# Kernel optimization log

Measured on AMD Instinct MI355X. Metric: run time of the kernel, lower is better.

## Reference

```python
import jax, jax.numpy as jnp
import numpy as np


def setup_inputs() -> dict:
    key = jax.random.key(0)
    k1, k2, k3, k4, k5 = jax.random.split(key, 5)
    B, C, H, W = 8, 256, 64, 64
    Cp = C // 8  # query/key channels
    x = jax.random.normal(k1, (B, C, H, W), dtype=jnp.float32)
    # 1x1 conv weights (bias=False in the module), spectral norm treated as a fixed weight scale
    Wq = jax.random.normal(k2, (Cp, C), dtype=jnp.float32) * 0.05
    Wk = jax.random.normal(k3, (Cp, C), dtype=jnp.float32) * 0.05
    Wv = jax.random.normal(k4, (C, C), dtype=jnp.float32) * 0.05
    gamma = jax.random.normal(k5, (1,), dtype=jnp.float32)
    return {"x": x, "Wq": Wq, "Wk": Wk, "Wv": Wv, "gamma": gamma}


def reference(x, Wq, Wk, Wv, gamma):
    B, C, H, W = x.shape
    xf = x.reshape(B, C, H * W)  # (B, C, N)
    # ConvLayer = 1x1 conv (no bias) followed by ReLU
    f = jax.nn.relu(jnp.einsum('oc,bcn->bon', Wq, xf))  # (B, C', N)
    g = jax.nn.relu(jnp.einsum('oc,bcn->bon', Wk, xf))  # (B, C', N)
    h = jax.nn.relu(jnp.einsum('oc,bcn->bon', Wv, xf))  # (B, C, N)
    # beta = softmax(f^T g, dim=1): normalize over the FIRST N axis (faithful to source)
    scores = jnp.einsum('bcn,bcm->bnm', f, g)  # (B, N, N)
    beta = jax.nn.softmax(scores, axis=1)
    o = gamma * jnp.einsum('bcn,bnm->bcm', h, beta) + xf  # (B, C, N)
    return o.reshape(B, C, H, W)
```

## Files before the change

kernel.cpp:

```cpp
#include <hip/hip_runtime.h>


typedef __attribute__((ext_vector_type(8))) short bf16x8;
typedef __attribute__((ext_vector_type(4))) float f32x4;
typedef __attribute__((ext_vector_type(4))) unsigned short us4;

#define LOG2E 1.44269504088896f

static __device__ __forceinline__ unsigned short f2bf(float x) {
    union { float f; unsigned u; } v; v.f = x;
    unsigned r = v.u + 0x7FFFu + ((v.u >> 16) & 1u);
    return (unsigned short)(r >> 16);
}
static __device__ __forceinline__ float bf2f(unsigned short u) {
    union { unsigned u; float f; } v; v.u = ((unsigned)u) << 16;
    return v.f;
}

__global__ __launch_bounds__(256) void wconv_kernel(
    const float* __restrict__ Wq, const float* __restrict__ Wk,
    const float* __restrict__ Wv, unsigned short* __restrict__ wq,
    unsigned short* __restrict__ wk, unsigned short* __restrict__ wv)
{
    const int i = blockIdx.x * 256 + threadIdx.x;
    if (i < 8192)            wq[i] = f2bf(Wq[i] * LOG2E);
    else if (i < 16384)      wk[i - 8192] = f2bf(Wk[i - 8192]);
    else                     wv[i - 16384] = f2bf(Wv[i - 16384]);
}

#define XPITCH 264
#define HPITCH 72
__global__ __launch_bounds__(256, 2) void producer_kernel(
    const float* __restrict__ x, const unsigned short* __restrict__ wq,
    const unsigned short* __restrict__ wk, const unsigned short* __restrict__ wv,
    unsigned short* __restrict__ f_t, unsigned short* __restrict__ g_t,
    unsigned short* __restrict__ h_bf, float* __restrict__ normg,
    float* __restrict__ pmax)
{
    __shared__ unsigned short xh_s[256 * HPITCH];
    __shared__ unsigned short fg_s[4 * 2 * 512];

    const int tid  = threadIdx.x;
    const int w    = tid >> 6;
    const int lane = tid & 63;
    const int q    = lane >> 4;
    const int r    = lane & 15;
    const int b    = blockIdx.x & 7;
    const int nt   = blockIdx.x >> 3;
    const int n0   = nt << 6;
    const size_t bN = (size_t)b << 12;
    const f32x4 zero = {0.f, 0.f, 0.f, 0.f};

#pragma unroll
    for (int jj = 0; jj < 4; jj++) {
        const int task = jj * 256 + tid;
        const int n4 = task & 15;
        const int c4 = task >> 4;
        float va[4][4];
#pragma unroll
        for (int i = 0; i < 4; i++) {
            const f32x4 v = __builtin_nontemporal_load(
                (const f32x4*)(x + ((size_t)b << 20)
                               + (size_t)(c4 * 4 + i) * 4096 + n0) + n4);
            va[i][0] = v.x; va[i][1] = v.y; va[i][2] = v.z; va[i][3] = v.w;
        }
#pragma unroll
        for (int i = 0; i < 4; i++) {
            us4 t;
            t.x = f2bf(va[0][i]); t.y = f2bf(va[1][i]);
            t.z = f2bf(va[2][i]); t.w = f2bf(va[3][i]);
            *(us4*)(xh_s + (n4 * 4 + i) * XPITCH + c4 * 4) = t;
        }
    }
    __syncthreads();

    f32x4 acch[4][4];
    f32x4 accf[2], accg[2];
#pragma unroll
    for (int cs = 0; cs < 4; cs++)
#pragma unroll
        for (int ns = 0; ns < 4; ns++) acch[cs][ns] = zero;
    accf[0] = accf[1] = accg[0] = accg[1] = zero;

    for (int ks = 0; ks < 8; ks++) {
        const int kof = ks * 32 + q * 8;
        bf16x8 av[4], aq[2], ak[2];
#pragma unroll
        for (int cs = 0; cs < 4; cs++)
            av[cs] = *(const bf16x8*)(wv + (size_t)(w * 64 + cs * 16 + r) * 256 + kof);
#pragma unroll
        for (int ms = 0; ms < 2; ms++) {
            aq[ms] = *(const bf16x8*)(wq + (size_t)(ms * 16 + r) * 256 + kof);
            ak[ms] = *(const bf16x8*)(wk + (size_t)(ms * 16 + r) * 256 + kof);
        }
#pragma unroll
        for (int ns = 0; ns < 4; ns++) {
            const bf16x8 bx = *(const bf16x8*)(xh_s + (ns * 16 + r) * XPITCH + kof);
#pragma unroll
            for (int cs = 0; cs < 4; cs++)
                acch[cs][ns] = __builtin_amdgcn_mfma_f32_16x16x32_bf16(av[cs], bx, acch[cs][ns], 0, 0, 0);
            if (ns == w) {
#pragma unroll
                for (int ms = 0; ms < 2; ms++) {
                    accf[ms] = __builtin_amdgcn_mfma_f32_16x16x32_bf16(aq[ms], bx, accf[ms], 0, 0, 0);
                    accg[ms] = __builtin_amdgcn_mfma_f32_16x16x32_bf16(ak[ms], bx, accg[ms], 0, 0, 0);
                }
            }
        }
    }

    unsigned short* lf = fg_s + w * 1024;
    unsigned short* lg = lf + 512;
#pragma unroll
    for (int ms = 0; ms < 2; ms++)
#pragma unroll
        for (int reg = 0; reg < 4; reg++) {
            lf[r * 32 + ms * 16 + q * 4 + reg] = f2bf(fmaxf(accf[ms][reg], 0.f));
            lg[r * 32 + ms * 16 + q * 4 + reg] = f2bf(fmaxf(accg[ms][reg], 0.f));
        }
    const bf16x8 ffrag = *(const bf16x8*)(lf + r * 32 + q * 8);
    const bf16x8 gfrag = *(const bf16x8*)(lg + r * 32 + q * 8);
    *(bf16x8*)(f_t + ((bN + n0 + w * 16 + r) << 5) + q * 8) = ffrag;
    *(bf16x8*)(g_t + ((bN + n0 + w * 16 + r) << 5) + q * 8) = gfrag;

    float nf2 = 0.f, ng2 = 0.f;
#pragma unroll
    for (int i = 0; i < 8; i++) {
        const float fv = bf2f(((unsigned short*)&ffrag)[i]);
        const float gv = bf2f(((unsigned short*)&gfrag)[i]);
        nf2 += fv * fv; ng2 += gv * gv;
    }
    nf2 += __shfl_xor(nf2, 16); nf2 += __shfl_xor(nf2, 32);
    ng2 += __shfl_xor(ng2, 16); ng2 += __shfl_xor(ng2, 32);
    if (q == 0) normg[bN + n0 + w * 16 + r] = sqrtf(ng2);
    float nf = sqrtf(nf2);
#pragma unroll
    for (int off = 1; off < 16; off <<= 1) nf = fmaxf(nf, __shfl_xor(nf, off));
    if (lane == 0) pmax[(b << 8) + nt * 4 + w] = nf;

    __syncthreads();
#pragma unroll
    for (int cs = 0; cs < 4; cs++)
#pragma unroll
        for (int ns = 0; ns < 4; ns++)
#pragma unroll
            for (int reg = 0; reg < 4; reg++)
                xh_s[(w * 64 + cs * 16 + q * 4 + reg) * HPITCH + ns * 16 + r] =
                    f2bf(fmaxf(acch[cs][ns][reg], 0.f));
    __syncthreads();
    const size_t hdst = ((size_t)(b * 64 + nt)) << 14;
#pragma unroll
    for (int p = 0; p < 8; p++) {
        const int c = p * 32 + (tid >> 3);
        const int k = tid & 7;
        *(bf16x8*)(h_bf + hdst + c * 64 + k * 8) =
            *(const bf16x8*)(xh_s + c * HPITCH + k * 8);
    }
}

__global__ __launch_bounds__(256, 2) void attn_kernel(
    const unsigned short* __restrict__ f_t, const unsigned short* __restrict__ g_t,
    const unsigned short* __restrict__ h_bf, const float* __restrict__ x,
    const float* __restrict__ gamma, const float* __restrict__ normg,
    const float* __restrict__ pmax, float* __restrict__ out)
{
    __shared__ unsigned short p_s[3][64 * 64];
    __shared__ float red_l[4][64];
    __shared__ float sLi[64];

    const int tid  = threadIdx.x;
    const int w    = tid >> 6;
    const int lane = tid & 63;
    const int q    = lane >> 4;
    const int r    = lane & 15;
    const int b    = blockIdx.x & 7;
    const int m0   = (blockIdx.x >> 3) << 6;

    const size_t bN = (size_t)b << 12;
    const int c0 = w << 6;

    float pv = pmax[(b << 8) + lane];
    pv = fmaxf(pv, pmax[(b << 8) + 64 + lane]);
    pv = fmaxf(pv, pmax[(b << 8) + 128 + lane]);
    pv = fmaxf(pv, pmax[(b << 8) + 192 + lane]);
#pragma unroll
    for (int off = 1; off < 64; off <<= 1) pv = fmaxf(pv, __shfl_xor(pv, off));
    const float mnf = pv;

    bf16x8 bg[4];
    float nMh[4];
#pragma unroll
    for (int ms = 0; ms < 4; ms++) {
        bg[ms] = *(const bf16x8*)(g_t + ((bN + m0 + ms * 16 + r) << 5) + (q << 3));
        nMh[ms] = -(mnf * normg[bN + m0 + ms * 16 + r] * 1.0002f);
    }

    f32x4 acc[4][4];
    const f32x4 zero = {0.f, 0.f, 0.f, 0.f};
#pragma unroll
    for (int cs = 0; cs < 4; cs++)
#pragma unroll
        for (int ms = 0; ms < 4; ms++) acc[cs][ms] = zero;
    float lt[4] = {0.f, 0.f, 0.f, 0.f};

    const int wkey = r & 7;
    const int wchunkoff = (((((w << 1) + (q >> 1)) ^ wkey) << 3)) + ((q & 1) << 2);
    const int rkoff0 = ((q ^ wkey) << 3);
    const int rkoff1 = (((4 + q) ^ wkey) << 3);

    auto ldf = [&](int t) {
        return *(const bf16x8*)(f_t + ((bN + (t << 6) + (w << 4) + r) << 5) + (q << 3));
    };
    auto produce = [&](const bf16x8 af, unsigned short* pb) {
#pragma unroll
        for (int ms = 0; ms < 4; ms++) {
            f32x4 ci; ci[0] = ci[1] = ci[2] = ci[3] = nMh[ms];
            const f32x4 sv = __builtin_amdgcn_mfma_f32_16x16x32_bf16(af, bg[ms], ci, 0, 0, 0);
            const float e0 = __builtin_amdgcn_exp2f(sv[0]);
            const float e1 = __builtin_amdgcn_exp2f(sv[1]);
            const float e2 = __builtin_amdgcn_exp2f(sv[2]);
            const float e3 = __builtin_amdgcn_exp2f(sv[3]);
            lt[ms] += (e0 + e1) + (e2 + e3);
            uint2 pk;
            pk.x = __builtin_amdgcn_perm(__float_as_uint(e1), __float_as_uint(e0), 0x07060302u);
            pk.y = __builtin_amdgcn_perm(__float_as_uint(e3), __float_as_uint(e2), 0x07060302u);
            *(uint2*)(pb + ((ms * 16 + r) << 6) + wchunkoff) = pk;
        }
    };

    bf16x8 afn = ldf(0);
    produce(afn, p_s[0]);
    afn = ldf(1);

    int sr = 0, sw = 1;
    for (int t = 0; t < 64; t++) {
        __syncthreads();
        const unsigned short* hb = h_bf + (((size_t)(b * 64 + t)) << 14);
        bf16x8 ah[8];
#pragma unroll
        for (int cs = 0; cs < 4; cs++) {
            const unsigned short* hp = hb + ((c0 + cs * 16 + r) << 6) + (q << 3);
            ah[cs * 2]     = *(const bf16x8*)(hp);
            ah[cs * 2 + 1] = *(const bf16x8*)(hp + 32);
        }
        if (t < 63) {
            const bf16x8 afc = afn;
            if (t < 62) afn = ldf(t + 2);
            produce(afc, p_s[sw]);
        }
        const unsigned short* pb = p_s[sr];
        bf16x8 bp[4][2];
#pragma unroll
        for (int ms = 0; ms < 4; ms++) {
            bp[ms][0] = *(const bf16x8*)(pb + ((ms * 16 + r) << 6) + rkoff0);
            bp[ms][1] = *(const bf16x8*)(pb + ((ms * 16 + r) << 6) + rkoff1);
        }
#pragma unroll
        for (int ch = 0; ch < 2; ch++)
#pragma unroll
            for (int cs = 0; cs < 4; cs++)
#pragma unroll
                for (int ms = 0; ms < 4; ms++)
                    acc[cs][ms] = __builtin_amdgcn_mfma_f32_16x16x32_bf16(
                        ah[cs * 2 + ch], bp[ms][ch], acc[cs][ms], 0, 0, 0);
        sr = sw;
        sw = (sw == 2) ? 0 : sw + 1;
    }

#pragma unroll
    for (int ms = 0; ms < 4; ms++) {
        lt[ms] += __shfl_xor(lt[ms], 16);
        lt[ms] += __shfl_xor(lt[ms], 32);
    }
    __syncthreads();
    if (q == 0)
#pragma unroll
        for (int ms = 0; ms < 4; ms++) red_l[w][ms * 16 + r] = lt[ms];
    __syncthreads();
    if (tid < 64)
        sLi[tid] = 1.f / (red_l[0][tid] + red_l[1][tid] + red_l[2][tid] + red_l[3][tid]);
    __syncthreads();

    const float gm = gamma[0];
#pragma unroll
    for (int cs = 0; cs < 4; cs++) {
#pragma unroll
        for (int ms = 0; ms < 4; ms++) {
            const float gl = gm * sLi[ms * 16 + r];
#pragma unroll
            for (int reg = 0; reg < 4; reg++) {
                const int c = c0 + cs * 16 + q * 4 + reg;
                const size_t a = (((size_t)b * 256 + c) << 12) + m0 + ms * 16 + r;
                const float xv = __builtin_nontemporal_load(x + a);
                __builtin_nontemporal_store(gl * acc[cs][ms][reg] + xv, out + a);
            }
        }
    }
}

extern "C" void kernel_launch(void* const* d_in, const int* in_sizes, int n_in,
                              void* d_out, int out_size, void* d_ws, size_t ws_size,
                              hipStream_t stream) {
    const float* x     = (const float*)d_in[0];
    const float* Wq    = (const float*)d_in[1];
    const float* Wk    = (const float*)d_in[2];
    const float* Wv    = (const float*)d_in[3];
    const float* gamma = (const float*)d_in[4];
    float* out = (float*)d_out;

    char* ws = (char*)d_ws;
    unsigned short* f_t  = (unsigned short*)ws;
    unsigned short* g_t  = (unsigned short*)(ws + (2u << 20));
    unsigned short* h_bf = (unsigned short*)(ws + (4u << 20));
    float*          ng   = (float*)(ws + (20u << 20));
    float*          pmx  = (float*)(ws + (20u << 20) + (1u << 17));
    unsigned short* wq   = (unsigned short*)(ws + (21u << 20));
    unsigned short* wk   = wq + 8192;
    unsigned short* wv   = wk + 8192;

    wconv_kernel<<<dim3(320), 256, 0, stream>>>(Wq, Wk, Wv, wq, wk, wv);
    producer_kernel<<<dim3(512), 256, 0, stream>>>(x, wq, wk, wv, f_t, g_t, h_bf, ng, pmx);
    attn_kernel<<<dim3(512), 256, 0, stream>>>(f_t, g_t, h_bf, x, gamma, ng, pmx, out);
}
```

Measured before the change: 250.6 us.

## Use 512-thread attention blocks with 128-row key tiles per iteration

The attention kernel now runs 8 waves per block. Each wave owns 32 output channels instead of 64, and each loop iteration processes a 128-row key tile, which halves the number of iterations and barriers. The P tile in shared memory doubles to 64x128 with a new XOR swizzle, and the accumulator registers per thread are halved so more waves can be resident. In exchange, more threads share each barrier, LDS use per block grows, and each h tile is loaded by more waves.

```diff
diff --git a/kernel.cpp b/kernel.cpp
--- a/kernel.cpp
+++ b/kernel.cpp
@@ -158,14 +158,14 @@
     }
 }
 
-__global__ __launch_bounds__(256, 2) void attn_kernel(
+__global__ __launch_bounds__(512, 4) void attn_kernel(
     const unsigned short* __restrict__ f_t, const unsigned short* __restrict__ g_t,
     const unsigned short* __restrict__ h_bf, const float* __restrict__ x,
     const float* __restrict__ gamma, const float* __restrict__ normg,
     const float* __restrict__ pmax, float* __restrict__ out)
 {
-    __shared__ unsigned short p_s[3][64 * 64];
-    __shared__ float red_l[4][64];
+    __shared__ unsigned short p_s[3][64 * 128];
+    __shared__ float red_l[8][64];
     __shared__ float sLi[64];
 
     const int tid  = threadIdx.x;
@@ -177,7 +177,7 @@
     const int m0   = (blockIdx.x >> 3) << 6;
 
     const size_t bN = (size_t)b << 12;
-    const int c0 = w << 6;
+    const int c0 = w << 5;
 
     float pv = pmax[(b << 8) + lane];
     pv = fmaxf(pv, pmax[(b << 8) + 64 + lane]);
@@ -195,21 +195,20 @@
         nMh[ms] = -(mnf * normg[bN + m0 + ms * 16 + r] * 1.0002f);
     }
 
-    f32x4 acc[4][4];
+    f32x4 acc[2][4];
     const f32x4 zero = {0.f, 0.f, 0.f, 0.f};
 #pragma unroll
-    for (int cs = 0; cs < 4; cs++)
+    for (int cs = 0; cs < 2; cs++)
 #pragma unroll
         for (int ms = 0; ms < 4; ms++) acc[cs][ms] = zero;
     float lt[4] = {0.f, 0.f, 0.f, 0.f};
 
-    const int wkey = r & 7;
-    const int wchunkoff = (((((w << 1) + (q >> 1)) ^ wkey) << 3)) + ((q & 1) << 2);
-    const int rkoff0 = ((q ^ wkey) << 3);
-    const int rkoff1 = (((4 + q) ^ wkey) << 3);
+    const int wchunk = (w << 1) + (q >> 1);
+    const int wphys  = (wchunk & 8) | ((wchunk ^ r) & 7);
+    const int woff   = (wphys << 3) + ((q & 1) << 2);
 
     auto ldf = [&](int t) {
-        return *(const bf16x8*)(f_t + ((bN + (t << 6) + (w << 4) + r) << 5) + (q << 3));
+        return *(const bf16x8*)(f_t + ((bN + (t << 7) + (w << 4) + r) << 5) + (q << 3));
     };
     auto produce = [&](const bf16x8 af, unsigned short* pb) {
 #pragma unroll
@@ -224,7 +223,7 @@
             uint2 pk;
             pk.x = __builtin_amdgcn_perm(__float_as_uint(e1), __float_as_uint(e0), 0x07060302u);
             pk.y = __builtin_amdgcn_perm(__float_as_uint(e3), __float_as_uint(e2), 0x07060302u);
-            *(uint2*)(pb + ((ms * 16 + r) << 6) + wchunkoff) = pk;
+            *(uint2*)(pb + ((ms * 16 + r) << 7) + woff) = pk;
         }
     };
 
@@ -233,36 +232,39 @@
     afn = ldf(1);
 
     int sr = 0, sw = 1;
-    for (int t = 0; t < 64; t++) {
+    for (int t = 0; t < 32; t++) {
         __syncthreads();
-        const unsigned short* hb = h_bf + (((size_t)(b * 64 + t)) << 14);
-        bf16x8 ah[8];
-#pragma unroll
-        for (int cs = 0; cs < 4; cs++) {
-            const unsigned short* hp = hb + ((c0 + cs * 16 + r) << 6) + (q << 3);
-            ah[cs * 2]     = *(const bf16x8*)(hp);
-            ah[cs * 2 + 1] = *(const bf16x8*)(hp + 32);
-        }
-        if (t < 63) {
+        bf16x8 ah[2][4];
+#pragma unroll
+        for (int ch = 0; ch < 4; ch++) {
+            const unsigned short* hb =
+                h_bf + (((size_t)(b * 64 + t * 2 + (ch >> 1))) << 14) + ((ch & 1) << 5) + (q << 3);
+#pragma unroll
+            for (int cs = 0; cs < 2; cs++)
+                ah[cs][ch] = *(const bf16x8*)(hb + ((c0 + cs * 16 + r) << 6));
+        }
+        if (t < 31) {
             const bf16x8 afc = afn;
-            if (t < 62) afn = ldf(t + 2);
+            if (t < 30) afn = ldf(t + 2);
             produce(afc, p_s[sw]);
         }
         const unsigned short* pb = p_s[sr];
-        bf16x8 bp[4][2];
-#pragma unroll
-        for (int ms = 0; ms < 4; ms++) {
-            bp[ms][0] = *(const bf16x8*)(pb + ((ms * 16 + r) << 6) + rkoff0);
-            bp[ms][1] = *(const bf16x8*)(pb + ((ms * 16 + r) << 6) + rkoff1);
-        }
-#pragma unroll
-        for (int ch = 0; ch < 2; ch++)
-#pragma unroll
-            for (int cs = 0; cs < 4; cs++)
+#pragma unroll
+        for (int ch = 0; ch < 4; ch++) {
+            bf16x8 bp[4];
+#pragma unroll
+            for (int ms = 0; ms < 4; ms++) {
+                const int idx  = (ch << 2) + q;
+                const int phys = (idx & 8) | ((idx ^ r) & 7);
+                bp[ms] = *(const bf16x8*)(pb + ((ms * 16 + r) << 7) + (phys << 3));
+            }
+#pragma unroll
+            for (int cs = 0; cs < 2; cs++)
 #pragma unroll
                 for (int ms = 0; ms < 4; ms++)
                     acc[cs][ms] = __builtin_amdgcn_mfma_f32_16x16x32_bf16(
-                        ah[cs * 2 + ch], bp[ms][ch], acc[cs][ms], 0, 0, 0);
+                        ah[cs][ch], bp[ms], acc[cs][ms], 0, 0, 0);
+        }
         sr = sw;
         sw = (sw == 2) ? 0 : sw + 1;
     }
@@ -277,13 +279,17 @@
 #pragma unroll
         for (int ms = 0; ms < 4; ms++) red_l[w][ms * 16 + r] = lt[ms];
     __syncthreads();
-    if (tid < 64)
-        sLi[tid] = 1.f / (red_l[0][tid] + red_l[1][tid] + red_l[2][tid] + red_l[3][tid]);
+    if (tid < 64) {
+        float L = 0.f;
+#pragma unroll
+        for (int ww = 0; ww < 8; ww++) L += red_l[ww][tid];
+        sLi[tid] = 1.f / L;
+    }
     __syncthreads();
 
     const float gm = gamma[0];
 #pragma unroll
-    for (int cs = 0; cs < 4; cs++) {
+    for (int cs = 0; cs < 2; cs++) {
 #pragma unroll
         for (int ms = 0; ms < 4; ms++) {
             const float gl = gm * sLi[ms * 16 + r];
@@ -320,5 +326,5 @@
 
     wconv_kernel<<<dim3(320), 256, 0, stream>>>(Wq, Wk, Wv, wq, wk, wv);
     producer_kernel<<<dim3(512), 256, 0, stream>>>(x, wq, wk, wv, f_t, g_t, h_bf, ng, pmx);
-    attn_kernel<<<dim3(512), 256, 0, stream>>>(f_t, g_t, h_bf, x, gamma, ng, pmx, out);
-}
+    attn_kernel<<<dim3(512), 512, 0, stream>>>(f_t, g_t, h_bf, x, gamma, ng, pmx, out);
+}
```

After: 249.5 us. No clear change (-0.5%).
